# Kernel optimization log

Hardware: AMD Instinct MI355X
Metric: run time of the kernel (lower is better)

## Reference

```python
import jax, jax.numpy as jnp
import numpy as np

B, C, HID, H, W = 32, 1024, 512, 56, 56

def setup_inputs() -> dict:
    key = jax.random.key(0)
    ks = jax.random.split(key, 8)
    s = 0.02
    return {
        "x":  jax.random.normal(ks[0], (B, C, H, W), dtype=jnp.float32),
        "W1": jax.random.normal(ks[1], (C, HID), dtype=jnp.float32) * s,  # mlp Linear(C->hidden), no bias
        "W2": jax.random.normal(ks[2], (HID, C), dtype=jnp.float32) * s,  # mlp Linear(hidden->C), no bias
        "WA": jax.random.normal(ks[3], (C, H), dtype=jnp.float32) * s,    # fc_A weight (transposed)
        "bA": jax.random.normal(ks[4], (H,), dtype=jnp.float32) * s,
        "WB": jax.random.normal(ks[5], (C, W), dtype=jnp.float32) * s,    # fc_B weight (transposed)
        "bB": jax.random.normal(ks[6], (W,), dtype=jnp.float32) * s,
    }

def reference(x, W1, W2, WA, bA, WB, bB):
    # Global average pool over spatial dims: (B, C)
    y = jnp.mean(x, axis=(2, 3))
    # MLP with exact (erf) GELU; dropout is identity in eval mode
    h = jax.nn.gelu(y @ W1, approximate=False)          # (B, HID)
    yp = jax.nn.gelu(h @ W2, approximate=False)          # (B, C)
    # Original replicates yp across C channels before fc_A/fc_B, so every
    # channel's attention map is identical: compute once, broadcast.
    A = yp @ WA + bA                                     # (B, H)
    Bv = yp @ WB + bB                                    # (B, W)
    attn = jax.nn.sigmoid(A[:, None, :, None] * Bv[:, None, None, :])  # (B, 1, H, W)
    return jnp.broadcast_to(attn, (x.shape[0], x.shape[1], A.shape[1], Bv.shape[1]))
```

## Files before the change

kernel.cpp:

```cpp
#include <hip/hip_runtime.h>
#include <math.h>

#define BATCH 32
#define NC    1024
#define NHID  512
#define NH    56
#define NW    56
#define HWSZ  3136
#define HW4   784

typedef float nfloat4 __attribute__((ext_vector_type(4)));

__device__ __forceinline__ float gelu_exact(float x) {
    return 0.5f * x * (1.0f + erff(x * 0.7071067811865476f));
}

__global__ __launch_bounds__(256) void gap_kernel(const float* __restrict__ x,
                                                  float* __restrict__ y) {
    const int row  = (blockIdx.x << 2) | (threadIdx.x >> 6);
    const int lane = threadIdx.x & 63;
    const nfloat4* xr = (const nfloat4*)(x + (size_t)row * HWSZ);

    float s = 0.f;
#pragma unroll
    for (int it = 0; it < 12; ++it) {
        nfloat4 v = __builtin_nontemporal_load(xr + lane + (it << 6));
        s += (v.x + v.y) + (v.z + v.w);
    }
    if (lane < 16) {
        nfloat4 v = __builtin_nontemporal_load(xr + 768 + lane);
        s += (v.x + v.y) + (v.z + v.w);
    }
#pragma unroll
    for (int off = 32; off > 0; off >>= 1) s += __shfl_down(s, off);
    if (lane == 0) y[row] = s * (1.0f / 3136.0f);
}

__global__ __launch_bounds__(256) void fc1_kernel(const float* __restrict__ y,
                                                  const float* __restrict__ W1,
                                                  float* __restrict__ h) {
    const int jc = blockIdx.x;
    const int b  = blockIdx.y;
    const int t  = threadIdx.x;

    __shared__ float   sy[NC];
    __shared__ nfloat4 part[256];
    __shared__ nfloat4 spart[64];
    for (int i = t; i < NC; i += 256) sy[i] = y[b * NC + i];
    __syncthreads();

    const int lane8 = t & 7;
    const int j0 = jc * 32 + lane8 * 4;
    const int ks = (t >> 3) * 32;

    nfloat4 acc0 = {0.f, 0.f, 0.f, 0.f};
    nfloat4 acc1 = {0.f, 0.f, 0.f, 0.f};
    const float* wbase = W1 + (size_t)ks * NHID + j0;
#pragma unroll 8
    for (int c = 0; c < 32; c += 2) {
        nfloat4 w0 = *(const nfloat4*)(wbase + (size_t)(c + 0) * NHID);
        nfloat4 w1 = *(const nfloat4*)(wbase + (size_t)(c + 1) * NHID);
        acc0 += sy[ks + c + 0] * w0;
        acc1 += sy[ks + c + 1] * w1;
    }
    part[t] = acc0 + acc1;
    __syncthreads();
    if (t < 64) spart[t] = part[t] + part[t + 64] + part[t + 128] + part[t + 192];
    __syncthreads();
    if (t < 8) {
        nfloat4 s = spart[t];
#pragma unroll
        for (int g = 1; g < 8; ++g) s += spart[g * 8 + t];
        float* hp = h + b * NHID + jc * 32 + t * 4;
        hp[0] = gelu_exact(s.x);
        hp[1] = gelu_exact(s.y);
        hp[2] = gelu_exact(s.z);
        hp[3] = gelu_exact(s.w);
    }
}

__global__ __launch_bounds__(256) void fc2_kernel(const float* __restrict__ h,
                                                  const float* __restrict__ W2,
                                                  float* __restrict__ yp) {
    const int cc = blockIdx.x;
    const int b  = blockIdx.y;
    const int t  = threadIdx.x;

    __shared__ float   sh[NHID];
    __shared__ nfloat4 part[256];
    __shared__ nfloat4 spart[64];
    for (int i = t; i < NHID; i += 256) sh[i] = h[b * NHID + i];
    __syncthreads();

    const int lane8 = t & 7;
    const int c0 = cc * 32 + lane8 * 4;
    const int js = (t >> 3) * 16;

    nfloat4 acc0 = {0.f, 0.f, 0.f, 0.f};
    nfloat4 acc1 = {0.f, 0.f, 0.f, 0.f};
    const float* wbase = W2 + (size_t)js * NC + c0;
#pragma unroll 8
    for (int jj = 0; jj < 16; jj += 2) {
        nfloat4 w0 = *(const nfloat4*)(wbase + (size_t)(jj + 0) * NC);
        nfloat4 w1 = *(const nfloat4*)(wbase + (size_t)(jj + 1) * NC);
        acc0 += sh[js + jj + 0] * w0;
        acc1 += sh[js + jj + 1] * w1;
    }
    part[t] = acc0 + acc1;
    __syncthreads();
    if (t < 64) spart[t] = part[t] + part[t + 64] + part[t + 128] + part[t + 192];
    __syncthreads();
    if (t < 8) {
        nfloat4 s = spart[t];
#pragma unroll
        for (int g = 1; g < 8; ++g) s += spart[g * 8 + t];
        float* pp = yp + b * NC + cc * 32 + t * 4;
        pp[0] = gelu_exact(s.x);
        pp[1] = gelu_exact(s.y);
        pp[2] = gelu_exact(s.z);
        pp[3] = gelu_exact(s.w);
    }
}

__global__ __launch_bounds__(512) void ab_kernel(
    const float* __restrict__ yp, const float* __restrict__ WA,
    const float* __restrict__ bA, const float* __restrict__ WB,
    const float* __restrict__ bB, float* __restrict__ AB) {
    const int b = blockIdx.x;
    const int t = threadIdx.x;

    __shared__ float   sp[NC];
    __shared__ nfloat4 partA[512];
    __shared__ nfloat4 partB[512];
    for (int i = t; i < NC; i += 512) sp[i] = yp[b * NC + i];
    __syncthreads();

    const int grp    = t >> 4;
    const int lane16 = t & 15;
    const int ks     = grp * 32;
    nfloat4 accA = {0.f, 0.f, 0.f, 0.f};
    nfloat4 accB = {0.f, 0.f, 0.f, 0.f};
    if (lane16 < 14) {
        const nfloat4* wa = (const nfloat4*)WA + (size_t)ks * 14 + lane16;
        const nfloat4* wb = (const nfloat4*)WB + (size_t)ks * 14 + lane16;
#pragma unroll 8
        for (int c = 0; c < 32; ++c) {
            const float sv = sp[ks + c];
            accA += sv * wa[(size_t)c * 14];
            accB += sv * wb[(size_t)c * 14];
        }
    }
    partA[t] = accA;
    partB[t] = accB;
    __syncthreads();
    if (t < 16) {
        nfloat4 s = partA[t];
#pragma unroll
        for (int g = 1; g < 32; ++g) s += partA[g * 16 + t];
        if (t < 14) {
            const int i0 = t * 4;
            AB[b * 128 + i0 + 0] = bA[i0 + 0] + s.x;
            AB[b * 128 + i0 + 1] = bA[i0 + 1] + s.y;
            AB[b * 128 + i0 + 2] = bA[i0 + 2] + s.z;
            AB[b * 128 + i0 + 3] = bA[i0 + 3] + s.w;
        }
    } else if (t < 32) {
        const int l = t - 16;
        nfloat4 s = partB[l];
#pragma unroll
        for (int g = 1; g < 32; ++g) s += partB[g * 16 + l];
        if (l < 14) {
            const int i0 = l * 4;
            AB[b * 128 + 64 + i0 + 0] = bB[i0 + 0] + s.x;
            AB[b * 128 + 64 + i0 + 1] = bB[i0 + 1] + s.y;
            AB[b * 128 + 64 + i0 + 2] = bB[i0 + 2] + s.z;
            AB[b * 128 + 64 + i0 + 3] = bB[i0 + 3] + s.w;
        }
    }
}

__global__ __launch_bounds__(256) void bcast_kernel(const float* __restrict__ AB,
                                                    float* __restrict__ out) {
    const int blk = blockIdx.x;
    const int b = blk >> 6;
    const int cchunk = blk & 63;
    const int t = threadIdx.x;

    __shared__ float sA[NH];
    __shared__ float sB[NW];
    __shared__ nfloat4 smap[HW4 + 64];
    if (t < NH) sA[t] = AB[b * 128 + t];
    else if (t >= 64 && t < 64 + NW) sB[t - 64] = AB[b * 128 + t];
    __syncthreads();

    for (int idx = t; idx < HW4 + 64; idx += 256) {
        const int p  = (idx >= HW4) ? idx - HW4 : idx;
        const int r  = p / 14;
        const int cb = (p - r * 14) * 4;
        const float a = sA[r];
        nfloat4 q;
        q.x = 1.0f / (1.0f + expf(-(a * sB[cb + 0])));
        q.y = 1.0f / (1.0f + expf(-(a * sB[cb + 1])));
        q.z = 1.0f / (1.0f + expf(-(a * sB[cb + 2])));
        q.w = 1.0f / (1.0f + expf(-(a * sB[cb + 3])));
        smap[idx] = q;
    }
    __syncthreads();

    const int w    = t >> 6;
    const int lane = t & 63;
    nfloat4* op = (nfloat4*)out +
                  ((size_t)b * NC + (size_t)cchunk * 16 + (size_t)w * 4) * HW4;
    int pos = 0;
#pragma unroll 7
    for (int it = 0; it < 49; ++it) {
        __builtin_nontemporal_store(smap[pos + lane], &op[it * 64 + lane]);
        pos += 64;
        if (pos >= HW4) pos -= HW4;
    }
}

extern "C" void kernel_launch(void* const* d_in, const int* in_sizes, int n_in,
                              void* d_out, int out_size, void* d_ws, size_t ws_size,
                              hipStream_t stream) {
    const float* x  = (const float*)d_in[0];
    const float* W1 = (const float*)d_in[1];
    const float* W2 = (const float*)d_in[2];
    const float* WA = (const float*)d_in[3];
    const float* bA = (const float*)d_in[4];
    const float* WB = (const float*)d_in[5];
    const float* bB = (const float*)d_in[6];
    float* out = (float*)d_out;

    float* y  = (float*)d_ws;
    float* yp = y;
    float* h  = y + BATCH * NC;
    float* AB = h + BATCH * NHID;

    gap_kernel<<<BATCH * NC / 4, 256, 0, stream>>>(x, y);
    fc1_kernel<<<dim3(NHID / 32, BATCH), 256, 0, stream>>>(y, W1, h);
    fc2_kernel<<<dim3(NC / 32, BATCH), 256, 0, stream>>>(h, W2, yp);
    ab_kernel<<<BATCH, 512, 0, stream>>>(yp, WA, bA, WB, bB, AB);
    bcast_kernel<<<BATCH * (NC / 16), 256, 0, stream>>>(AB, out);
}
```

Baseline: 162.1 us.

## Fuse fc1, fc2 and A/B projections into one persistent kernel with grid barriers

Replaces the three small MLP/projection launches with one 512-block kernel that steps through fc1, fc2 and the A/B projections, separated by atomic-counter grid barriers. The A/B projection is also split across 16 channel segments per batch, with a final reduction stage, so more blocks share that work. The aim is to remove launch gaps and the single-block-per-batch bottleneck of the old A/B kernel. In exchange it adds a memset launch and spin-wait barriers, and it assumes all 512 blocks are co-resident, which risks deadlock if they are not.

```diff
diff --git a/kernel.cpp b/kernel.cpp
--- a/kernel.cpp
+++ b/kernel.cpp
@@ -36,146 +36,142 @@
     if (lane == 0) y[row] = s * (1.0f / 3136.0f);
 }
 
-__global__ __launch_bounds__(256) void fc1_kernel(const float* __restrict__ y,
-                                                  const float* __restrict__ W1,
-                                                  float* __restrict__ h) {
-    const int jc = blockIdx.x;
-    const int b  = blockIdx.y;
-    const int t  = threadIdx.x;
-
-    __shared__ float   sy[NC];
+__device__ __forceinline__ void grid_barrier(unsigned* cnt, unsigned expected) {
+    __syncthreads();
+    if (threadIdx.x == 0) {
+        __threadfence();
+        atomicAdd(cnt, 1u);
+        while (__hip_atomic_load(cnt, __ATOMIC_ACQUIRE,
+                                 __HIP_MEMORY_SCOPE_AGENT) < expected) {
+            __builtin_amdgcn_s_sleep(2);
+        }
+    }
+    __syncthreads();
+}
+
+__global__ __launch_bounds__(256, 2) void mlp_fused_kernel(
+    const float* __restrict__ y,  const float* __restrict__ W1,
+    const float* __restrict__ W2, const float* __restrict__ WA,
+    const float* __restrict__ bA, const float* __restrict__ WB,
+    const float* __restrict__ bB, float* __restrict__ h,
+    float* __restrict__ yp, float* __restrict__ partial,
+    float* __restrict__ AB, unsigned* __restrict__ bar) {
+    const int blk = blockIdx.x;
+    const int t   = threadIdx.x;
+    const unsigned NBLK = gridDim.x;
+
+    __shared__ float   sbuf[NC];
     __shared__ nfloat4 part[256];
     __shared__ nfloat4 spart[64];
-    for (int i = t; i < NC; i += 256) sy[i] = y[b * NC + i];
-    __syncthreads();
-
-    const int lane8 = t & 7;
-    const int j0 = jc * 32 + lane8 * 4;
-    const int ks = (t >> 3) * 32;
-
-    nfloat4 acc0 = {0.f, 0.f, 0.f, 0.f};
-    nfloat4 acc1 = {0.f, 0.f, 0.f, 0.f};
-    const float* wbase = W1 + (size_t)ks * NHID + j0;
+
+    {
+        const int jc = blk & 15;
+        const int b  = blk >> 4;
+        for (int i = t; i < NC; i += 256) sbuf[i] = y[b * NC + i];
+        __syncthreads();
+
+        const int lane8 = t & 7;
+        const int j0 = jc * 32 + lane8 * 4;
+        const int ks = (t >> 3) * 32;
+        nfloat4 acc0 = {0.f, 0.f, 0.f, 0.f};
+        nfloat4 acc1 = {0.f, 0.f, 0.f, 0.f};
+        const float* wbase = W1 + (size_t)ks * NHID + j0;
 #pragma unroll 8
-    for (int c = 0; c < 32; c += 2) {
-        nfloat4 w0 = *(const nfloat4*)(wbase + (size_t)(c + 0) * NHID);
-        nfloat4 w1 = *(const nfloat4*)(wbase + (size_t)(c + 1) * NHID);
-        acc0 += sy[ks + c + 0] * w0;
-        acc1 += sy[ks + c + 1] * w1;
-    }
-    part[t] = acc0 + acc1;
-    __syncthreads();
-    if (t < 64) spart[t] = part[t] + part[t + 64] + part[t + 128] + part[t + 192];
-    __syncthreads();
-    if (t < 8) {
-        nfloat4 s = spart[t];
-#pragma unroll
-        for (int g = 1; g < 8; ++g) s += spart[g * 8 + t];
-        float* hp = h + b * NHID + jc * 32 + t * 4;
-        hp[0] = gelu_exact(s.x);
-        hp[1] = gelu_exact(s.y);
-        hp[2] = gelu_exact(s.z);
-        hp[3] = gelu_exact(s.w);
-    }
-}
-
-__global__ __launch_bounds__(256) void fc2_kernel(const float* __restrict__ h,
-                                                  const float* __restrict__ W2,
-                                                  float* __restrict__ yp) {
-    const int cc = blockIdx.x;
-    const int b  = blockIdx.y;
-    const int t  = threadIdx.x;
-
-    __shared__ float   sh[NHID];
-    __shared__ nfloat4 part[256];
-    __shared__ nfloat4 spart[64];
-    for (int i = t; i < NHID; i += 256) sh[i] = h[b * NHID + i];
-    __syncthreads();
-
-    const int lane8 = t & 7;
-    const int c0 = cc * 32 + lane8 * 4;
-    const int js = (t >> 3) * 16;
-
-    nfloat4 acc0 = {0.f, 0.f, 0.f, 0.f};
-    nfloat4 acc1 = {0.f, 0.f, 0.f, 0.f};
-    const float* wbase = W2 + (size_t)js * NC + c0;
+        for (int c = 0; c < 32; c += 2) {
+            nfloat4 w0 = *(const nfloat4*)(wbase + (size_t)(c + 0) * NHID);
+            nfloat4 w1 = *(const nfloat4*)(wbase + (size_t)(c + 1) * NHID);
+            acc0 += sbuf[ks + c + 0] * w0;
+            acc1 += sbuf[ks + c + 1] * w1;
+        }
+        part[t] = acc0 + acc1;
+        __syncthreads();
+        if (t < 64) spart[t] = part[t] + part[t + 64] + part[t + 128] + part[t + 192];
+        __syncthreads();
+        if (t < 8) {
+            nfloat4 s = spart[t];
+#pragma unroll
+            for (int g = 1; g < 8; ++g) s += spart[g * 8 + t];
+            float* hp = h + b * NHID + jc * 32 + t * 4;
+            hp[0] = gelu_exact(s.x);
+            hp[1] = gelu_exact(s.y);
+            hp[2] = gelu_exact(s.z);
+            hp[3] = gelu_exact(s.w);
+        }
+    }
+    grid_barrier(&bar[0], NBLK);
+
+    {
+        const int u0 = blk * 2;
+        const int b  = u0 >> 5;
+        for (int i = t; i < NHID; i += 256) sbuf[i] = h[b * NHID + i];
+        __syncthreads();
+
+#pragma unroll
+        for (int uu = 0; uu < 2; ++uu) {
+            const int cc = (u0 + uu) & 31;
+            const int lane8 = t & 7;
+            const int c0 = cc * 32 + lane8 * 4;
+            const int js = (t >> 3) * 16;
+            nfloat4 acc0 = {0.f, 0.f, 0.f, 0.f};
+            nfloat4 acc1 = {0.f, 0.f, 0.f, 0.f};
+            const float* wbase = W2 + (size_t)js * NC + c0;
 #pragma unroll 8
-    for (int jj = 0; jj < 16; jj += 2) {
-        nfloat4 w0 = *(const nfloat4*)(wbase + (size_t)(jj + 0) * NC);
-        nfloat4 w1 = *(const nfloat4*)(wbase + (size_t)(jj + 1) * NC);
-        acc0 += sh[js + jj + 0] * w0;
-        acc1 += sh[js + jj + 1] * w1;
-    }
-    part[t] = acc0 + acc1;
-    __syncthreads();
-    if (t < 64) spart[t] = part[t] + part[t + 64] + part[t + 128] + part[t + 192];
-    __syncthreads();
-    if (t < 8) {
-        nfloat4 s = spart[t];
-#pragma unroll
-        for (int g = 1; g < 8; ++g) s += spart[g * 8 + t];
-        float* pp = yp + b * NC + cc * 32 + t * 4;
-        pp[0] = gelu_exact(s.x);
-        pp[1] = gelu_exact(s.y);
-        pp[2] = gelu_exact(s.z);
-        pp[3] = gelu_exact(s.w);
-    }
-}
-
-__global__ __launch_bounds__(512) void ab_kernel(
-    const float* __restrict__ yp, const float* __restrict__ WA,
-    const float* __restrict__ bA, const float* __restrict__ WB,
-    const float* __restrict__ bB, float* __restrict__ AB) {
-    const int b = blockIdx.x;
-    const int t = threadIdx.x;
-
-    __shared__ float   sp[NC];
-    __shared__ nfloat4 partA[512];
-    __shared__ nfloat4 partB[512];
-    for (int i = t; i < NC; i += 512) sp[i] = yp[b * NC + i];
-    __syncthreads();
-
-    const int grp    = t >> 4;
-    const int lane16 = t & 15;
-    const int ks     = grp * 32;
-    nfloat4 accA = {0.f, 0.f, 0.f, 0.f};
-    nfloat4 accB = {0.f, 0.f, 0.f, 0.f};
-    if (lane16 < 14) {
-        const nfloat4* wa = (const nfloat4*)WA + (size_t)ks * 14 + lane16;
-        const nfloat4* wb = (const nfloat4*)WB + (size_t)ks * 14 + lane16;
-#pragma unroll 8
-        for (int c = 0; c < 32; ++c) {
-            const float sv = sp[ks + c];
-            accA += sv * wa[(size_t)c * 14];
-            accB += sv * wb[(size_t)c * 14];
-        }
-    }
-    partA[t] = accA;
-    partB[t] = accB;
-    __syncthreads();
-    if (t < 16) {
-        nfloat4 s = partA[t];
-#pragma unroll
-        for (int g = 1; g < 32; ++g) s += partA[g * 16 + t];
-        if (t < 14) {
-            const int i0 = t * 4;
-            AB[b * 128 + i0 + 0] = bA[i0 + 0] + s.x;
-            AB[b * 128 + i0 + 1] = bA[i0 + 1] + s.y;
-            AB[b * 128 + i0 + 2] = bA[i0 + 2] + s.z;
-            AB[b * 128 + i0 + 3] = bA[i0 + 3] + s.w;
-        }
-    } else if (t < 32) {
-        const int l = t - 16;
-        nfloat4 s = partB[l];
-#pragma unroll
-        for (int g = 1; g < 32; ++g) s += partB[g * 16 + l];
-        if (l < 14) {
-            const int i0 = l * 4;
-            AB[b * 128 + 64 + i0 + 0] = bB[i0 + 0] + s.x;
-            AB[b * 128 + 64 + i0 + 1] = bB[i0 + 1] + s.y;
-            AB[b * 128 + 64 + i0 + 2] = bB[i0 + 2] + s.z;
-            AB[b * 128 + 64 + i0 + 3] = bB[i0 + 3] + s.w;
-        }
+            for (int jj = 0; jj < 16; jj += 2) {
+                nfloat4 w0 = *(const nfloat4*)(wbase + (size_t)(jj + 0) * NC);
+                nfloat4 w1 = *(const nfloat4*)(wbase + (size_t)(jj + 1) * NC);
+                acc0 += sbuf[js + jj + 0] * w0;
+                acc1 += sbuf[js + jj + 1] * w1;
+            }
+            part[t] = acc0 + acc1;
+            __syncthreads();
+            if (t < 64) spart[t] = part[t] + part[t + 64] + part[t + 128] + part[t + 192];
+            __syncthreads();
+            if (t < 8) {
+                nfloat4 s = spart[t];
+#pragma unroll
+                for (int g = 1; g < 8; ++g) s += spart[g * 8 + t];
+                float* pp = yp + b * NC + cc * 32 + t * 4;
+                pp[0] = gelu_exact(s.x);
+                pp[1] = gelu_exact(s.y);
+                pp[2] = gelu_exact(s.z);
+                pp[3] = gelu_exact(s.w);
+            }
+            __syncthreads();
+        }
+    }
+    grid_barrier(&bar[1], NBLK);
+
+    {
+        const int b   = blk >> 4;
+        const int seg = blk & 15;
+        const int ks  = seg * 64;
+        if (t < 64) sbuf[t] = yp[b * NC + ks + t];
+        __syncthreads();
+        if (t < 112) {
+            const bool isA = t < 56;
+            const int  i   = isA ? t : t - 56;
+            const float* w = (isA ? WA : WB) + (size_t)ks * 56 + i;
+            float a0 = 0.f, a1 = 0.f, a2 = 0.f, a3 = 0.f;
+#pragma unroll 4
+            for (int c = 0; c < 64; c += 4) {
+                a0 += sbuf[c + 0] * w[(size_t)(c + 0) * 56];
+                a1 += sbuf[c + 1] * w[(size_t)(c + 1) * 56];
+                a2 += sbuf[c + 2] * w[(size_t)(c + 2) * 56];
+                a3 += sbuf[c + 3] * w[(size_t)(c + 3) * 56];
+            }
+            partial[((size_t)b * 16 + seg) * 112 + t] = (a0 + a1) + (a2 + a3);
+        }
+    }
+    grid_barrier(&bar[2], NBLK);
+
+    if (blk < BATCH && t < 112) {
+        const int b = blk;
+        float s = (t < 56) ? bA[t] : bB[t - 56];
+#pragma unroll
+        for (int g = 0; g < 16; ++g)
+            s += partial[((size_t)b * 16 + g) * 112 + t];
+        const int idx = (t < 56) ? t : (t + 8);
+        AB[b * 128 + idx] = s;
     }
 }
 
@@ -232,14 +228,16 @@
     const float* bB = (const float*)d_in[6];
     float* out = (float*)d_out;
 
-    float* y  = (float*)d_ws;
-    float* yp = y;
-    float* h  = y + BATCH * NC;
-    float* AB = h + BATCH * NHID;
-
+    float* y       = (float*)d_ws;
+    float* h       = y + BATCH * NC;
+    float* yp      = h + BATCH * NHID;
+    float* AB      = yp + BATCH * NC;
+    float* partial = AB + BATCH * 128;
+    unsigned* bar  = (unsigned*)(partial + BATCH * 16 * 112);
+
+    hipMemsetAsync(bar, 0, 16, stream);
     gap_kernel<<<BATCH * NC / 4, 256, 0, stream>>>(x, y);
-    fc1_kernel<<<dim3(NHID / 32, BATCH), 256, 0, stream>>>(y, W1, h);
-    fc2_kernel<<<dim3(NC / 32, BATCH), 256, 0, stream>>>(h, W2, yp);
-    ab_kernel<<<BATCH, 512, 0, stream>>>(yp, WA, bA, WB, bB, AB);
+    mlp_fused_kernel<<<512, 256, 0, stream>>>(y, W1, W2, WA, bA, WB, bB,
+                                              h, yp, partial, AB, bar);
     bcast_kernel<<<BATCH * (NC / 16), 256, 0, stream>>>(AB, out);
 }
```

After: 303.4 us. 1.87x slower.

## Fuse fc_A/fc_B projection into fc2 via atomics and coarsen broadcast blocks

Applied to the files above, without the earlier changes.

Removes the separate ab_kernel launch. Each fc2 block now applies GELU to its 32-channel slice of yp in shared memory, multiplies it by the matching rows of WA and WB, and atomically adds the partial sums into AB. fc1 pre-seeds AB with the biases. The broadcast kernel also moves from 2048 blocks of 16 channels each to 512 blocks of 64 channels each, so the sigmoid map is computed fewer times. The cost is float atomics, which make the summation order nondeterministic, and fewer blocks for the store-bound broadcast.

```diff
diff --git a/kernel.cpp b/kernel.cpp
--- a/kernel.cpp
+++ b/kernel.cpp
@@ -38,7 +38,10 @@
 
 __global__ __launch_bounds__(256) void fc1_kernel(const float* __restrict__ y,
                                                   const float* __restrict__ W1,
-                                                  float* __restrict__ h) {
+                                                  const float* __restrict__ bA,
+                                                  const float* __restrict__ bB,
+                                                  float* __restrict__ h,
+                                                  float* __restrict__ AB) {
     const int jc = blockIdx.x;
     const int b  = blockIdx.y;
     const int t  = threadIdx.x;
@@ -77,11 +80,17 @@
         hp[2] = gelu_exact(s.z);
         hp[3] = gelu_exact(s.w);
     }
-}
-
-__global__ __launch_bounds__(256) void fc2_kernel(const float* __restrict__ h,
-                                                  const float* __restrict__ W2,
-                                                  float* __restrict__ yp) {
+    if (jc == 0) {
+        if (t < NH)                         AB[b * 128 + t]      = bA[t];
+        else if (t >= 64 && t < 64 + NW)    AB[b * 128 + t]      = bB[t - 64];
+    }
+}
+
+__global__ __launch_bounds__(256) void fc2ab_kernel(const float* __restrict__ h,
+                                                    const float* __restrict__ W2,
+                                                    const float* __restrict__ WA,
+                                                    const float* __restrict__ WB,
+                                                    float* __restrict__ AB) {
     const int cc = blockIdx.x;
     const int b  = blockIdx.y;
     const int t  = threadIdx.x;
@@ -89,6 +98,7 @@
     __shared__ float   sh[NHID];
     __shared__ nfloat4 part[256];
     __shared__ nfloat4 spart[64];
+    __shared__ float   ypl[32];
     for (int i = t; i < NHID; i += 256) sh[i] = h[b * NHID + i];
     __syncthreads();
 
@@ -112,78 +122,36 @@
     __syncthreads();
     if (t < 8) {
         nfloat4 s = spart[t];
-#pragma unroll
+        #pragma unroll
         for (int g = 1; g < 8; ++g) s += spart[g * 8 + t];
-        float* pp = yp + b * NC + cc * 32 + t * 4;
-        pp[0] = gelu_exact(s.x);
-        pp[1] = gelu_exact(s.y);
-        pp[2] = gelu_exact(s.z);
-        pp[3] = gelu_exact(s.w);
-    }
-}
-
-__global__ __launch_bounds__(512) void ab_kernel(
-    const float* __restrict__ yp, const float* __restrict__ WA,
-    const float* __restrict__ bA, const float* __restrict__ WB,
-    const float* __restrict__ bB, float* __restrict__ AB) {
-    const int b = blockIdx.x;
-    const int t = threadIdx.x;
-
-    __shared__ float   sp[NC];
-    __shared__ nfloat4 partA[512];
-    __shared__ nfloat4 partB[512];
-    for (int i = t; i < NC; i += 512) sp[i] = yp[b * NC + i];
-    __syncthreads();
-
-    const int grp    = t >> 4;
-    const int lane16 = t & 15;
-    const int ks     = grp * 32;
-    nfloat4 accA = {0.f, 0.f, 0.f, 0.f};
-    nfloat4 accB = {0.f, 0.f, 0.f, 0.f};
-    if (lane16 < 14) {
-        const nfloat4* wa = (const nfloat4*)WA + (size_t)ks * 14 + lane16;
-        const nfloat4* wb = (const nfloat4*)WB + (size_t)ks * 14 + lane16;
-#pragma unroll 8
-        for (int c = 0; c < 32; ++c) {
-            const float sv = sp[ks + c];
-            accA += sv * wa[(size_t)c * 14];
-            accB += sv * wb[(size_t)c * 14];
+        ypl[t * 4 + 0] = gelu_exact(s.x);
+        ypl[t * 4 + 1] = gelu_exact(s.y);
+        ypl[t * 4 + 2] = gelu_exact(s.z);
+        ypl[t * 4 + 3] = gelu_exact(s.w);
+    }
+    __syncthreads();
+
+    if (t < 112) {
+        const bool isA = t < 56;
+        const int  i   = isA ? t : t - 56;
+        const float* w = (isA ? WA : WB) + (size_t)(cc * 32) * 56 + i;
+        float a0 = 0.f, a1 = 0.f, a2 = 0.f, a3 = 0.f;
+#pragma unroll 4
+        for (int c = 0; c < 32; c += 4) {
+            a0 += ypl[c + 0] * w[(size_t)(c + 0) * 56];
+            a1 += ypl[c + 1] * w[(size_t)(c + 1) * 56];
+            a2 += ypl[c + 2] * w[(size_t)(c + 2) * 56];
+            a3 += ypl[c + 3] * w[(size_t)(c + 3) * 56];
         }
-    }
-    partA[t] = accA;
-    partB[t] = accB;
-    __syncthreads();
-    if (t < 16) {
-        nfloat4 s = partA[t];
-#pragma unroll
-        for (int g = 1; g < 32; ++g) s += partA[g * 16 + t];
-        if (t < 14) {
-            const int i0 = t * 4;
-            AB[b * 128 + i0 + 0] = bA[i0 + 0] + s.x;
-            AB[b * 128 + i0 + 1] = bA[i0 + 1] + s.y;
-            AB[b * 128 + i0 + 2] = bA[i0 + 2] + s.z;
-            AB[b * 128 + i0 + 3] = bA[i0 + 3] + s.w;
-        }
-    } else if (t < 32) {
-        const int l = t - 16;
-        nfloat4 s = partB[l];
-#pragma unroll
-        for (int g = 1; g < 32; ++g) s += partB[g * 16 + l];
-        if (l < 14) {
-            const int i0 = l * 4;
-            AB[b * 128 + 64 + i0 + 0] = bB[i0 + 0] + s.x;
-            AB[b * 128 + 64 + i0 + 1] = bB[i0 + 1] + s.y;
-            AB[b * 128 + 64 + i0 + 2] = bB[i0 + 2] + s.z;
-            AB[b * 128 + 64 + i0 + 3] = bB[i0 + 3] + s.w;
-        }
+        atomicAdd(&AB[b * 128 + (isA ? i : 64 + i)], (a0 + a1) + (a2 + a3));
     }
 }
 
 __global__ __launch_bounds__(256) void bcast_kernel(const float* __restrict__ AB,
                                                     float* __restrict__ out) {
     const int blk = blockIdx.x;
-    const int b = blk >> 6;
-    const int cchunk = blk & 63;
+    const int b = blk >> 4;
+    const int chunk = blk & 15;
     const int t = threadIdx.x;
 
     __shared__ float sA[NH];
@@ -210,10 +178,10 @@
     const int w    = t >> 6;
     const int lane = t & 63;
     nfloat4* op = (nfloat4*)out +
-                  ((size_t)b * NC + (size_t)cchunk * 16 + (size_t)w * 4) * HW4;
+                  ((size_t)b * NC + (size_t)chunk * 64 + (size_t)w * 16) * HW4;
     int pos = 0;
 #pragma unroll 7
-    for (int it = 0; it < 49; ++it) {
+    for (int it = 0; it < 196; ++it) {
         __builtin_nontemporal_store(smap[pos + lane], &op[it * 64 + lane]);
         pos += 64;
         if (pos >= HW4) pos -= HW4;
@@ -233,13 +201,11 @@
     float* out = (float*)d_out;
 
     float* y  = (float*)d_ws;
-    float* yp = y;
     float* h  = y + BATCH * NC;
     float* AB = h + BATCH * NHID;
 
     gap_kernel<<<BATCH * NC / 4, 256, 0, stream>>>(x, y);
-    fc1_kernel<<<dim3(NHID / 32, BATCH), 256, 0, stream>>>(y, W1, h);
-    fc2_kernel<<<dim3(NC / 32, BATCH), 256, 0, stream>>>(h, W2, yp);
-    ab_kernel<<<BATCH, 512, 0, stream>>>(yp, WA, bA, WB, bB, AB);
-    bcast_kernel<<<BATCH * (NC / 16), 256, 0, stream>>>(AB, out);
-}
+    fc1_kernel<<<dim3(16, BATCH), 256, 0, stream>>>(y, W1, bA, bB, h, AB);
+    fc2ab_kernel<<<dim3(32, BATCH), 256, 0, stream>>>(h, W2, WA, WB, AB);
+    bcast_kernel<<<512, 256, 0, stream>>>(AB, out);
+}
```

New measurement: 159.6 us, median of 2. No clear change (-1.6%).
